# Kernel tuning notes

Measured on AMD Instinct MI355X. Metric: run time of the kernel, lower is better.

## Reference

```python
import jax, jax.numpy as jnp
import numpy as np

B, S, D = 2, 4096, 512   # batch, seq_len, hidden_dim
H, E = 8, 64             # n_heads, head_dim


def setup_inputs() -> dict:
    key = jax.random.key(0)
    ks = jax.random.split(key, 14)
    s = 0.02  # init scale
    return {
        "x":  jax.random.normal(ks[0], (B, S, D), dtype=jnp.float32),
        # stacked per-head projection weights, stored as [H, in, out]
        "wq": jax.random.normal(ks[1], (H, D, E), dtype=jnp.float32) * s,
        "bq": jax.random.normal(ks[2], (H, E), dtype=jnp.float32) * s,
        "wk": jax.random.normal(ks[3], (H, D, E), dtype=jnp.float32) * s,
        "bk": jax.random.normal(ks[4], (H, E), dtype=jnp.float32) * s,
        "wv": jax.random.normal(ks[5], (H, D, E), dtype=jnp.float32) * s,
        "bv": jax.random.normal(ks[6], (H, E), dtype=jnp.float32) * s,
        "wo": jax.random.normal(ks[7], (H, E, D), dtype=jnp.float32) * s,
        "bo": jax.random.normal(ks[8], (H, D), dtype=jnp.float32) * s,
        # MLP: Linear(D,D) -> ReLU -> Linear(D,D), stored as [in, out]
        "w1": jax.random.normal(ks[9], (D, D), dtype=jnp.float32) * s,
        "b1": jax.random.normal(ks[10], (D,), dtype=jnp.float32) * s,
        "w2": jax.random.normal(ks[11], (D, D), dtype=jnp.float32) * s,
        "b2": jax.random.normal(ks[12], (D,), dtype=jnp.float32) * s,
    }


def reference(x, wq, bq, wk, bk, wv, bv, wo, bo, w1, b1, w2, b2):
    # Per-head projections, batched over heads: [B, H, S, E]
    q = jnp.einsum('bsd,hde->bhse', x, wq) + bq[None, :, None, :]
    k = jnp.einsum('bsd,hde->bhse', x, wk) + bk[None, :, None, :]
    v = jnp.einsum('bsd,hde->bhse', x, wv) + bv[None, :, None, :]
    scale = 1.0 / jnp.sqrt(jnp.asarray(q.shape[-1], q.dtype))
    scores = jnp.einsum('bhse,bhte->bhst', q, k) * scale  # [B,H,S,S]
    A = jax.nn.softmax(scores, axis=-1)
    ctx = jnp.einsum('bhst,bhte->bhse', A, v)             # [B,H,S,E]
    # w_o per head then sum over heads (each head adds its bias once)
    y = jnp.einsum('bhse,hed->bsd', ctx, wo) + jnp.sum(bo, axis=0)
    # MLP
    h = jax.nn.relu(y @ w1 + b1)
    return h @ w2 + b2
```

## Files before the change

### kernel.cpp

```cpp
#include <hip/hip_runtime.h>
#include <math.h>

#define Bsz 2
#define Sq  4096
#define Dm  512
#define Hn  8
#define Eh  64

typedef unsigned short u16;
typedef __attribute__((ext_vector_type(8))) short bf16x8;
typedef __attribute__((ext_vector_type(4))) short bf16x4;
typedef __attribute__((ext_vector_type(4))) float f32x4;
typedef __attribute__((ext_vector_type(4))) unsigned short u16x4;

#define KSCALE 0.18033688011112042f

__device__ __forceinline__ f32x4 mfma_16x16x16(bf16x4 a, bf16x4 b, f32x4 c) {
#if defined(__HIP_DEVICE_COMPILE__)
#if __has_builtin(__builtin_amdgcn_mfma_f32_16x16x16bf16_1k)
    return __builtin_amdgcn_mfma_f32_16x16x16bf16_1k(a, b, c, 0, 0, 0);
#else
    f32x4 d;
    asm volatile("v_mfma_f32_16x16x16_bf16 %0, %1, %2, %3"
                 : "=v"(d) : "v"(a), "v"(b), "v"(c));
    return d;
#endif
#else
    (void)a; (void)b;
    return c;
#endif
}

__device__ __forceinline__ u16 f2bf(float f) {
    unsigned int u = __float_as_uint(f);
    u += 0x7FFFu + ((u >> 16) & 1u);
    return (u16)(u >> 16);
}

__device__ __forceinline__ float fast_exp2(float x) {
#if defined(__HIP_DEVICE_COMPILE__) && __has_builtin(__builtin_amdgcn_exp2f)
    return __builtin_amdgcn_exp2f(x);
#else
    return exp2f(x);
#endif
}

__device__ __forceinline__ void async16(const u16* g, u16* l) {
    __builtin_amdgcn_global_load_lds(
        (const __attribute__((address_space(1))) void*)g,
        (__attribute__((address_space(3))) void*)l, 16, 0, 0);
}

template<int TN, int NT>
__device__ __forceinline__ void gemm_core(
    const u16* __restrict__ A, const u16* __restrict__ WT,
    int m0, int n0, u16* Ast, u16* Bst, f32x4 (&acc)[4][NT])
{
    const int tid  = threadIdx.x;
    const int lane = tid & 63, wid = tid >> 6;
    const int l15  = lane & 15, quad = lane >> 4;
    const int wm = wid >> 1, wn = wid & 1;

    for (int kt = 0; kt < Dm / 64; ++kt) {
        const int k0 = kt * 64;
        __syncthreads();
#pragma unroll
        for (int j = 0; j < 4; ++j) {
            int ci = wid * 256 + j * 64 + lane;
            int row = ci >> 3, c = (ci & 7) ^ (row & 7);
            async16(&A[(size_t)(m0 + row) * Dm + k0 + c * 8],
                    &Ast[(size_t)(wid * 256 + j * 64) * 8]);
        }
#pragma unroll
        for (int j = 0; j < TN / 32; ++j) {
            int ci = wid * (TN * 2) + j * 64 + lane;
            int row = ci >> 3, c = (ci & 7) ^ (row & 7);
            async16(&WT[(size_t)(n0 + row) * Dm + k0 + c * 8],
                    &Bst[(size_t)(wid * (TN * 2) + j * 64) * 8]);
        }
        __syncthreads();
#pragma unroll
        for (int ks = 0; ks < 2; ++ks) {
            bf16x8 af[4], bfr[NT];
#pragma unroll
            for (int mt = 0; mt < 4; ++mt) {
                int r = wm * 64 + mt * 16 + l15;
                af[mt] = *(const bf16x8*)&Ast[(r * 8 + ((ks * 4 + quad) ^ (r & 7))) * 8];
            }
#pragma unroll
            for (int nt = 0; nt < NT; ++nt) {
                int n = wn * (TN / 2) + nt * 16 + l15;
                bfr[nt] = *(const bf16x8*)&Bst[(n * 8 + ((ks * 4 + quad) ^ (n & 7))) * 8];
            }
#pragma unroll
            for (int mt = 0; mt < 4; ++mt)
#pragma unroll
                for (int nt = 0; nt < NT; ++nt)
                    acc[mt][nt] = __builtin_amdgcn_mfma_f32_16x16x32_bf16(
                        af[mt], bfr[nt], acc[mt][nt], 0, 0, 0);
        }
    }
}

__global__ __launch_bounds__(256) void prep_kernel(
    const float* __restrict__ x,
    const float* __restrict__ wq, const float* __restrict__ wk,
    const float* __restrict__ wv, const float* __restrict__ wo,
    const float* __restrict__ w1, const float* __restrict__ w2,
    const float* __restrict__ bo,
    u16* __restrict__ xb, u16* __restrict__ wqkvT, u16* __restrict__ woT,
    u16* __restrict__ w1T, u16* __restrict__ w2T, float* __restrict__ bo_s)
{
    const int seg = blockIdx.y, bx = blockIdx.x, tid = threadIdx.x;
    if (seg == 0) {
        const float4* xi = (const float4*)x;
        for (int i = bx * 256 + tid; i < (Bsz * Sq * Dm) / 4; i += 64 * 256) {
            float4 v = xi[i];
            u16x4 o = {f2bf(v.x), f2bf(v.y), f2bf(v.z), f2bf(v.w)};
            *(u16x4*)&xb[(size_t)i * 4] = o;
        }
        return;
    }
    if (seg == 7) {
        int d = bx * 256 + tid;
        if (d < Dm) {
            float s = 0.0f;
#pragma unroll
            for (int h = 0; h < Hn; ++h) s += bo[h * Dm + d];
            bo_s[d] = s;
        }
        return;
    }
    __shared__ float t[64][65];
    const float* src; u16* dst; int ld_in;
    if (seg <= 3) {
        const float* w = (seg == 1) ? wq : (seg == 2) ? wk : wv;
        int head = bx >> 3, kt = bx & 7;
        src = w + (size_t)head * Dm * Eh + (size_t)kt * 64 * 64;
        ld_in = 64;
        dst = wqkvT + ((size_t)((seg - 1) * 8 + head) * 64) * 512 + kt * 64;
    } else {
        const float* w = (seg == 4) ? wo : (seg == 5) ? w1 : w2;
        u16* dT = (seg == 4) ? woT : (seg == 5) ? w1T : w2T;
        int tr = bx >> 3, tc = bx & 7;
        src = w + (size_t)(tr * 64) * 512 + tc * 64;
        ld_in = 512;
        dst = dT + (size_t)(tc * 64) * 512 + tr * 64;
    }
#pragma unroll
    for (int it = 0; it < 16; ++it) {
        int idx = it * 256 + tid;
        int r = idx >> 6, c = idx & 63;
        t[r][c] = src[(size_t)r * ld_in + c];
    }
    __syncthreads();
#pragma unroll
    for (int it = 0; it < 4; ++it) {
        int idx = it * 256 + tid;
        int oc = idx >> 4, og = idx & 15;
        u16x4 o;
#pragma unroll
        for (int j = 0; j < 4; ++j) o[j] = f2bf(t[og * 4 + j][oc]);
        *(u16x4*)&dst[(size_t)oc * 512 + og * 4] = o;
    }
}

__global__ __launch_bounds__(256, 2) void qkv_gemm(
    const u16* __restrict__ xb, const u16* __restrict__ wqkvT,
    const float* __restrict__ bq, const float* __restrict__ bk,
    const float* __restrict__ bv,
    u16* __restrict__ qb, u16* __restrict__ kb, u16* __restrict__ vbT)
{
    __shared__ __align__(16) u16 Ast[128 * 64];
    __shared__ __align__(16) u16 Bst[64 * 64];
    const int proj = blockIdx.y >> 3, h = blockIdx.y & 7;
    const u16* WT = wqkvT + (size_t)blockIdx.y * 64 * 512;

    f32x4 acc[4][2];
#pragma unroll
    for (int i = 0; i < 4; ++i)
#pragma unroll
        for (int j = 0; j < 2; ++j) acc[i][j] = (f32x4)0.0f;

    gemm_core<64, 2>(xb, WT, blockIdx.x * 128, 0, Ast, Bst, acc);

    const int tid = threadIdx.x;
    const int lane = tid & 63, wid = tid >> 6;
    const int l15 = lane & 15, quad = lane >> 4;
    const int wm = wid >> 1, wn = wid & 1;
    const float* bias = (proj == 0) ? bq : (proj == 1) ? bk : bv;

    const int mbase = blockIdx.x * 128 + wm * 64;
    const int b = mbase >> 12;
    const int sbase = (mbase & (Sq - 1));
    const int bh = b * Hn + h;

#pragma unroll
    for (int mt = 0; mt < 4; ++mt)
#pragma unroll
        for (int nt = 0; nt < 2; ++nt) {
            int e = wn * 32 + nt * 16 + l15;
            float bval = bias[h * Eh + e];
            int s = sbase + mt * 16 + quad * 4;
            if (proj == 2) {
                u16x4 o;
#pragma unroll
                for (int r = 0; r < 4; ++r) o[r] = f2bf(acc[mt][nt][r] + bval);
                *(u16x4*)&vbT[((size_t)bh * Eh + e) * Sq + s] = o;
            } else if (proj == 1) {
                for (int r = 0; r < 4; ++r)
                    kb[((size_t)bh * Sq + s + r) * Eh + e] =
                        f2bf((acc[mt][nt][r] + bval) * KSCALE);
            } else {
                for (int r = 0; r < 4; ++r)
                    qb[((size_t)bh * Sq + s + r) * Eh + e] = f2bf(acc[mt][nt][r] + bval);
            }
        }
}

__global__ __launch_bounds__(256, 2) void attn_kernel(
    const u16* __restrict__ qb, const u16* __restrict__ kb,
    const u16* __restrict__ vbT, u16* __restrict__ ctxb)
{
    __shared__ __align__(16) u16 kst[2][128 * 64];
    __shared__ __align__(16) u16 vst[2][64 * 128];

    const int tid  = threadIdx.x;
    const int lane = tid & 63, wid = tid >> 6;
    const int l15  = lane & 15, quad = lane >> 4;
    const int bh = blockIdx.y;
    const int q0 = blockIdx.x * 128;
    const int b = bh >> 3, h = bh & 7;

    const u16* qg = qb + (size_t)bh * Sq * Eh;
    const u16* kg = kb + (size_t)bh * Sq * Eh;
    const u16* vg = vbT + (size_t)bh * Eh * Sq;

    int krow[4], kcol[4], vrow[4], vcol[4];
#pragma unroll
    for (int j = 0; j < 4; ++j) {
        int ci = wid * 256 + j * 64 + lane;
        krow[j] = ci >> 3;
        kcol[j] = (ci & 7) ^ (krow[j] & 7);
        vrow[j] = ci >> 4;
        int vc  = ci & 15;
        vcol[j] = (vc & 8) | ((vc & 7) ^ (vrow[j] & 7));
    }

    bf16x8 qf[2][2];
#pragma unroll
    for (int qt = 0; qt < 2; ++qt)
#pragma unroll
        for (int ks = 0; ks < 2; ++ks)
            qf[qt][ks] = *(const bf16x8*)&qg[(size_t)(q0 + wid * 32 + qt * 16 + l15) * Eh + ks * 32 + quad * 8];

    f32x4 O[4][2];
    float lp[2];
#pragma unroll
    for (int et = 0; et < 4; ++et)
#pragma unroll
        for (int qt = 0; qt < 2; ++qt) O[et][qt] = (f32x4)0.0f;
    lp[0] = lp[1] = 0.0f;

#pragma unroll
    for (int j = 0; j < 4; ++j) {
        async16(&kg[(size_t)krow[j] * Eh + kcol[j] * 8],
                &kst[0][(wid * 256 + j * 64) * 8]);
        async16(&vg[(size_t)vrow[j] * Sq + vcol[j] * 8],
                &vst[0][(wid * 256 + j * 64) * 8]);
    }

    for (int kt = 0; kt < Sq / 128; ++kt) {
        const int cur = kt & 1;
        __syncthreads();

        if (kt < Sq / 128 - 1) {
            const int t1 = (kt + 1) * 128;
#pragma unroll
            for (int j = 0; j < 4; ++j) {
                async16(&kg[(size_t)(t1 + krow[j]) * Eh + kcol[j] * 8],
                        &kst[cur ^ 1][(wid * 256 + j * 64) * 8]);
                async16(&vg[(size_t)vrow[j] * Sq + t1 + vcol[j] * 8],
                        &vst[cur ^ 1][(wid * 256 + j * 64) * 8]);
            }
        }

        const u16* kcur = kst[cur];
        const u16* vcur = vst[cur];

        bf16x4 pf[8][2];
#pragma unroll
        for (int half = 0; half < 2; ++half) {
            f32x4 S[4][2];
#pragma unroll
            for (int tt = 0; tt < 4; ++tt)
#pragma unroll
                for (int qt = 0; qt < 2; ++qt) S[tt][qt] = (f32x4)0.0f;
#pragma unroll
            for (int ks = 0; ks < 2; ++ks)
#pragma unroll
                for (int tt = 0; tt < 4; ++tt) {
                    int t = (half * 4 + tt) * 16 + l15;
                    bf16x8 kf = *(const bf16x8*)&kcur[t * 64 + ((ks * 4 + quad) ^ (t & 7)) * 8];
                    S[tt][0] = __builtin_amdgcn_mfma_f32_16x16x32_bf16(kf, qf[0][ks], S[tt][0], 0, 0, 0);
                    S[tt][1] = __builtin_amdgcn_mfma_f32_16x16x32_bf16(kf, qf[1][ks], S[tt][1], 0, 0, 0);
                }
#pragma unroll
            for (int tt = 0; tt < 4; ++tt)
#pragma unroll
                for (int qt = 0; qt < 2; ++qt)
#pragma unroll
                    for (int r = 0; r < 4; ++r) {
                        float p = fast_exp2(S[tt][qt][r]);
                        lp[qt] += p;
                        pf[half * 4 + tt][qt][r] = (short)(__float_as_uint(p) >> 16);
                    }
        }

#pragma unroll
        for (int et = 0; et < 4; ++et) {
            int e = et * 16 + l15;
#pragma unroll
            for (int ttg = 0; ttg < 8; ++ttg) {
                int c  = ttg * 2 + (quad >> 1);
                int gc = (c & 8) | ((c & 7) ^ (e & 7));
                bf16x4 vf = *(const bf16x4*)&vcur[e * 128 + gc * 8 + (quad & 1) * 4];
                O[et][0] = mfma_16x16x16(vf, pf[ttg][0], O[et][0]);
                O[et][1] = mfma_16x16x16(vf, pf[ttg][1], O[et][1]);
            }
        }
    }

#pragma unroll
    for (int qt = 0; qt < 2; ++qt) {
        float v = lp[qt];
        v += __shfl_xor(v, 16, 64);
        v += __shfl_xor(v, 32, 64);
        lp[qt] = v;
    }

#pragma unroll
    for (int qt = 0; qt < 2; ++qt) {
        const int qglob = q0 + wid * 32 + qt * 16 + l15;
        const float rl = 1.0f / lp[qt];
        u16* crow = ctxb + ((size_t)(b * Sq + qglob) * Hn + h) * Eh;
#pragma unroll
        for (int et = 0; et < 4; ++et) {
            u16x4 o;
#pragma unroll
            for (int r = 0; r < 4; ++r) o[r] = f2bf(O[et][qt][r] * rl);
            *(u16x4*)&crow[et * 16 + quad * 4] = o;
        }
    }
}

template<int MODE>
__global__ __launch_bounds__(256, 2) void gemmMN(
    const u16* __restrict__ A, const u16* __restrict__ WT,
    const float* __restrict__ bias, void* __restrict__ Cout)
{
    __shared__ __align__(16) u16 Ast[128 * 64];
    __shared__ __align__(16) u16 Bst[64 * 64];

    f32x4 acc[4][2];
#pragma unroll
    for (int i = 0; i < 4; ++i)
#pragma unroll
        for (int j = 0; j < 2; ++j) acc[i][j] = (f32x4)0.0f;

    gemm_core<64, 2>(A, WT, blockIdx.x * 128, blockIdx.y * 64, Ast, Bst, acc);

    const int tid = threadIdx.x;
    const int lane = tid & 63, wid = tid >> 6;
    const int l15 = lane & 15, quad = lane >> 4;
    const int m0 = blockIdx.x * 128 + (wid >> 1) * 64;
    const int n0 = blockIdx.y * 64 + (wid & 1) * 32;

#pragma unroll
    for (int mt = 0; mt < 4; ++mt)
#pragma unroll
        for (int nt = 0; nt < 2; ++nt) {
            int col = n0 + nt * 16 + l15;
            float bval = bias[col];
#pragma unroll
            for (int r = 0; r < 4; ++r) {
                int row = m0 + mt * 16 + quad * 4 + r;
                float v = acc[mt][nt][r] + bval;
                if (MODE == 1) v = fmaxf(v, 0.0f);
                if (MODE == 2) ((float*)Cout)[(size_t)row * Dm + col] = v;
                else           ((u16*)Cout)[(size_t)row * Dm + col] = f2bf(v);
            }
        }
}

extern "C" void kernel_launch(void* const* d_in, const int* in_sizes, int n_in,
                              void* d_out, int out_size, void* d_ws, size_t ws_size,
                              hipStream_t stream)
{
    const float* x  = (const float*)d_in[0];
    const float* wq = (const float*)d_in[1];
    const float* bq = (const float*)d_in[2];
    const float* wk = (const float*)d_in[3];
    const float* bk = (const float*)d_in[4];
    const float* wv = (const float*)d_in[5];
    const float* bv = (const float*)d_in[6];
    const float* wo = (const float*)d_in[7];
    const float* bo = (const float*)d_in[8];
    const float* w1 = (const float*)d_in[9];
    const float* b1 = (const float*)d_in[10];
    const float* w2 = (const float*)d_in[11];
    const float* b2 = (const float*)d_in[12];
    float* out = (float*)d_out;
    char* wsb = (char*)d_ws;

    const size_t MB = 1u << 20;
    u16*   xb    = (u16*)(wsb + 0);
    u16*   qb    = (u16*)(wsb + 8 * MB);
    u16*   kb    = (u16*)(wsb + 16 * MB);
    u16*   vbT   = (u16*)(wsb + 24 * MB);
    u16*   ctxb  = (u16*)(wsb + 32 * MB);
    u16*   ybuf  = (u16*)(wsb + 40 * MB);
    u16*   h1    = (u16*)(wsb + 48 * MB);
    u16*   wqkvT = (u16*)(wsb + 56 * MB);
    u16*   woT   = (u16*)(wsb + 58 * MB);
    u16*   w1T   = (u16*)(wsb + 59 * MB);
    u16*   w2T   = (u16*)(wsb + 60 * MB);
    float* bo_s  = (float*)(wsb + 61 * MB);

    prep_kernel<<<dim3(64, 8), 256, 0, stream>>>(
        x, wq, wk, wv, wo, w1, w2, bo, xb, wqkvT, woT, w1T, w2T, bo_s);
    qkv_gemm<<<dim3(Sq * Bsz / 128, 24), 256, 0, stream>>>(
        xb, wqkvT, bq, bk, bv, qb, kb, vbT);
    attn_kernel<<<dim3(Sq / 128, Bsz * Hn), 256, 0, stream>>>(qb, kb, vbT, ctxb);
    gemmMN<0><<<dim3(Bsz * Sq / 128, Dm / 64), 256, 0, stream>>>(ctxb, woT, bo_s, ybuf);
    gemmMN<1><<<dim3(Bsz * Sq / 128, Dm / 64), 256, 0, stream>>>(ybuf, w1T, b1, h1);
    gemmMN<2><<<dim3(Bsz * Sq / 128, Dm / 64), 256, 0, stream>>>(h1, w2T, b2, out);
}
```

Before: 244.7 us.

## Switch attention inner loop to 32x32x16 MFMA with in-register P layout swap

Rewrites the attention kernel's QK^T and PV products to use 32x32x16 bf16 MFMA tiles instead of 16x16 tiles. The softmax probabilities are packed with v_cvt_pk_bf16_f32 and rearranged across lane halves with v_permlane32_swap, so P feeds the second MFMA directly as an operand without LDS. Larger tiles mean fewer MFMA issues and fewer LDS fragment loads per unit of work. The trade-offs are more accumulator registers, a rounding conversion for P where the old code truncated, and reliance on gfx950-specific instructions.

```diff
diff --git a/kernel.cpp b/kernel.cpp
--- a/kernel.cpp
+++ b/kernel.cpp
@@ -9,27 +9,11 @@
 
 typedef unsigned short u16;
 typedef __attribute__((ext_vector_type(8))) short bf16x8;
-typedef __attribute__((ext_vector_type(4))) short bf16x4;
 typedef __attribute__((ext_vector_type(4))) float f32x4;
+typedef __attribute__((ext_vector_type(16))) float f32x16;
 typedef __attribute__((ext_vector_type(4))) unsigned short u16x4;
 
 #define KSCALE 0.18033688011112042f
-
-__device__ __forceinline__ f32x4 mfma_16x16x16(bf16x4 a, bf16x4 b, f32x4 c) {
-#if defined(__HIP_DEVICE_COMPILE__)
-#if __has_builtin(__builtin_amdgcn_mfma_f32_16x16x16bf16_1k)
-    return __builtin_amdgcn_mfma_f32_16x16x16bf16_1k(a, b, c, 0, 0, 0);
-#else
-    f32x4 d;
-    asm volatile("v_mfma_f32_16x16x16_bf16 %0, %1, %2, %3"
-                 : "=v"(d) : "v"(a), "v"(b), "v"(c));
-    return d;
-#endif
-#else
-    (void)a; (void)b;
-    return c;
-#endif
-}
 
 __device__ __forceinline__ u16 f2bf(float f) {
     unsigned int u = __float_as_uint(f);
@@ -43,6 +27,37 @@
 #else
     return exp2f(x);
 #endif
+}
+
+__device__ __forceinline__ f32x16 mfma_32x32x16(bf16x8 a, bf16x8 b, f32x16 c) {
+#if defined(__HIP_DEVICE_COMPILE__)
+    return __builtin_amdgcn_mfma_f32_32x32x16_bf16(a, b, c, 0, 0, 0);
+#else
+    (void)a; (void)b;
+    return c;
+#endif
+}
+
+__device__ __forceinline__ unsigned cvt_pk_bf16(float lo, float hi) {
+#if defined(__HIP_DEVICE_COMPILE__)
+    unsigned r;
+    asm("v_cvt_pk_bf16_f32 %0, %1, %2" : "=v"(r) : "v"(lo), "v"(hi));
+    return r;
+#else
+    return ((unsigned)f2bf(hi) << 16) | (unsigned)f2bf(lo);
+#endif
+}
+
+__device__ __forceinline__ void plane32_swap(unsigned &a, unsigned &b) {
+#if defined(__HIP_DEVICE_COMPILE__)
+    asm volatile("v_permlane32_swap_b32 %0, %1" : "+v"(a), "+v"(b));
+#endif
+}
+
+__device__ __forceinline__ bf16x8 frag_of(unsigned a, unsigned b, unsigned c, unsigned d) {
+    union { unsigned u[4]; bf16x8 v; } r;
+    r.u[0] = a; r.u[1] = b; r.u[2] = c; r.u[3] = d;
+    return r.v;
 }
 
 __device__ __forceinline__ void async16(const u16* g, u16* l) {
@@ -227,7 +242,7 @@
 
     const int tid  = threadIdx.x;
     const int lane = tid & 63, wid = tid >> 6;
-    const int l15  = lane & 15, quad = lane >> 4;
+    const int l31  = lane & 31, hh = lane >> 5;
     const int bh = blockIdx.y;
     const int q0 = blockIdx.x * 128;
     const int b = bh >> 3, h = bh & 7;
@@ -247,20 +262,18 @@
         vcol[j] = (vc & 8) | ((vc & 7) ^ (vrow[j] & 7));
     }
 
-    bf16x8 qf[2][2];
-#pragma unroll
-    for (int qt = 0; qt < 2; ++qt)
-#pragma unroll
-        for (int ks = 0; ks < 2; ++ks)
-            qf[qt][ks] = *(const bf16x8*)&qg[(size_t)(q0 + wid * 32 + qt * 16 + l15) * Eh + ks * 32 + quad * 8];
-
-    f32x4 O[4][2];
-    float lp[2];
-#pragma unroll
-    for (int et = 0; et < 4; ++et)
-#pragma unroll
-        for (int qt = 0; qt < 2; ++qt) O[et][qt] = (f32x4)0.0f;
-    lp[0] = lp[1] = 0.0f;
+    bf16x8 qf[4];
+    {
+        const u16* qrow = &qg[(size_t)(q0 + wid * 32 + l31) * Eh + hh * 8];
+#pragma unroll
+        for (int ks = 0; ks < 4; ++ks)
+            qf[ks] = *(const bf16x8*)&qrow[ks * 16];
+    }
+
+    f32x16 O[2];
+    O[0] = (f32x16)0.0f;
+    O[1] = (f32x16)0.0f;
+    float lp = 0.0f;
 
 #pragma unroll
     for (int j = 0; j < 4; ++j) {
@@ -270,6 +283,8 @@
                 &vst[0][(wid * 256 + j * 64) * 8]);
     }
 
+    const int t7 = l31 & 7;
+
     for (int kt = 0; kt < Sq / 128; ++kt) {
         const int cur = kt & 1;
         __syncthreads();
@@ -288,70 +303,60 @@
         const u16* kcur = kst[cur];
         const u16* vcur = vst[cur];
 
-        bf16x4 pf[8][2];
-#pragma unroll
-        for (int half = 0; half < 2; ++half) {
-            f32x4 S[4][2];
-#pragma unroll
-            for (int tt = 0; tt < 4; ++tt)
-#pragma unroll
-                for (int qt = 0; qt < 2; ++qt) S[tt][qt] = (f32x4)0.0f;
-#pragma unroll
-            for (int ks = 0; ks < 2; ++ks)
-#pragma unroll
-                for (int tt = 0; tt < 4; ++tt) {
-                    int t = (half * 4 + tt) * 16 + l15;
-                    bf16x8 kf = *(const bf16x8*)&kcur[t * 64 + ((ks * 4 + quad) ^ (t & 7)) * 8];
-                    S[tt][0] = __builtin_amdgcn_mfma_f32_16x16x32_bf16(kf, qf[0][ks], S[tt][0], 0, 0, 0);
-                    S[tt][1] = __builtin_amdgcn_mfma_f32_16x16x32_bf16(kf, qf[1][ks], S[tt][1], 0, 0, 0);
-                }
-#pragma unroll
-            for (int tt = 0; tt < 4; ++tt)
-#pragma unroll
-                for (int qt = 0; qt < 2; ++qt)
-#pragma unroll
-                    for (int r = 0; r < 4; ++r) {
-                        float p = fast_exp2(S[tt][qt][r]);
-                        lp[qt] += p;
-                        pf[half * 4 + tt][qt][r] = (short)(__float_as_uint(p) >> 16);
-                    }
-        }
-
-#pragma unroll
-        for (int et = 0; et < 4; ++et) {
-            int e = et * 16 + l15;
-#pragma unroll
-            for (int ttg = 0; ttg < 8; ++ttg) {
-                int c  = ttg * 2 + (quad >> 1);
-                int gc = (c & 8) | ((c & 7) ^ (e & 7));
-                bf16x4 vf = *(const bf16x4*)&vcur[e * 128 + gc * 8 + (quad & 1) * 4];
-                O[et][0] = mfma_16x16x16(vf, pf[ttg][0], O[et][0]);
-                O[et][1] = mfma_16x16x16(vf, pf[ttg][1], O[et][1]);
-            }
-        }
-    }
-
-#pragma unroll
-    for (int qt = 0; qt < 2; ++qt) {
-        float v = lp[qt];
-        v += __shfl_xor(v, 16, 64);
-        v += __shfl_xor(v, 32, 64);
-        lp[qt] = v;
-    }
-
-#pragma unroll
-    for (int qt = 0; qt < 2; ++qt) {
-        const int qglob = q0 + wid * 32 + qt * 16 + l15;
-        const float rl = 1.0f / lp[qt];
-        u16* crow = ctxb + ((size_t)(b * Sq + qglob) * Hn + h) * Eh;
-#pragma unroll
-        for (int et = 0; et < 4; ++et) {
+#pragma unroll
+        for (int tt = 0; tt < 4; ++tt) {
+            f32x16 S = (f32x16)0.0f;
+            const int trow = (tt * 32 + l31) * 64;
+#pragma unroll
+            for (int ks = 0; ks < 4; ++ks) {
+                bf16x8 kf = *(const bf16x8*)&kcur[trow + ((ks * 2 + hh) ^ t7) * 8];
+                S = mfma_32x32x16(kf, qf[ks], S);
+            }
+
+            unsigned px[8];
+#pragma unroll
+            for (int j = 0; j < 8; ++j) {
+                float p0 = fast_exp2(S[2 * j]);
+                float p1 = fast_exp2(S[2 * j + 1]);
+                lp += p0 + p1;
+                px[j] = cvt_pk_bf16(p0, p1);
+            }
+            plane32_swap(px[0], px[2]);
+            plane32_swap(px[1], px[3]);
+            plane32_swap(px[4], px[6]);
+            plane32_swap(px[5], px[7]);
+            bf16x8 f0 = frag_of(px[0], px[1], px[2], px[3]);
+            bf16x8 f1 = frag_of(px[4], px[5], px[6], px[7]);
+
+#pragma unroll
+            for (int et = 0; et < 2; ++et) {
+                const int erow = (et * 32 + l31) * 128;
+                int c0 = tt * 4 + hh;
+                int c1 = c0 + 2;
+                int g0 = (c0 & 8) | ((c0 & 7) ^ t7);
+                int g1 = (c1 & 8) | ((c1 & 7) ^ t7);
+                bf16x8 v0 = *(const bf16x8*)&vcur[erow + g0 * 8];
+                bf16x8 v1 = *(const bf16x8*)&vcur[erow + g1 * 8];
+                O[et] = mfma_32x32x16(v0, f0, O[et]);
+                O[et] = mfma_32x32x16(v1, f1, O[et]);
+            }
+        }
+    }
+
+    lp += __shfl_xor(lp, 32, 64);
+    const float rl = 1.0f / lp;
+
+    const int qglob = q0 + wid * 32 + l31;
+    u16* crow = ctxb + ((size_t)(b * Sq + qglob) * Hn + h) * Eh;
+#pragma unroll
+    for (int et = 0; et < 2; ++et)
+#pragma unroll
+        for (int g = 0; g < 4; ++g) {
             u16x4 o;
 #pragma unroll
-            for (int r = 0; r < 4; ++r) o[r] = f2bf(O[et][qt][r] * rl);
-            *(u16x4*)&crow[et * 16 + quad * 4] = o;
-        }
-    }
+            for (int i = 0; i < 4; ++i) o[i] = f2bf(O[et][g * 4 + i] * rl);
+            *(u16x4*)&crow[et * 32 + g * 8 + hh * 4] = o;
+        }
 }
 
 template<int MODE>
```

Measured after the change: 239.4 us. 1.02x faster.
